# Kernel tuning notes

Measured on AMD Instinct MI355X. Metric: run time of the kernel, lower is better.

## Reference

```python
import jax, jax.numpy as jnp
import numpy as np
from jax import lax

EPS = 1e-4

def _baseconv(x, w, g, b):
    # Conv (no bias) + folded BatchNorm (per-channel scale g, shift b) + SiLU
    k = w.shape[-1]
    pad = [((k - 1) // 2, (k - 1) // 2)] * 2
    y = lax.conv_general_dilated(x, w, (1, 1), pad,
                                 dimension_numbers=('NCHW', 'OIHW', 'NCHW'))
    y = y * g[None, :, None, None] + b[None, :, None, None]
    return y * jax.nn.sigmoid(y)  # SiLU

def _block_norm(x, s):
    # Divide each of the s*s spatial sub-blocks by its global mean (over B,C,h,w)
    B, C, H, W = x.shape
    h, w = H // s, W // s
    xb = x.reshape(B, C, s, h, s, w)
    m = xb.mean(axis=(0, 1, 3, 5), keepdims=True)  # (1,1,s,1,s,1) scalar per block
    return (xb / (m + EPS)).reshape(B, C, H, W)


def setup_inputs() -> dict:
    key = jax.random.key(0)
    ks = jax.random.split(key, 8)
    B, C, H, W = 4, 128, 256, 256
    d = {}
    d['x'] = jax.random.normal(ks[0], (B, C, H, W), dtype=jnp.float32)
    def conv_w(k, cout, cin, ksz):
        return jax.random.normal(k, (cout, cin, ksz, ksz), dtype=jnp.float32) * 0.02
    # fc1/fc2/fc3: 1x1 dim->dim for SagMean scales 1,2,4
    d['w1'] = conv_w(ks[1], C, C, 1); d['g1'] = jnp.ones((C,)); d['b1'] = jnp.zeros((C,))
    d['w2'] = conv_w(ks[2], C, C, 1); d['g2'] = jnp.ones((C,)); d['b2'] = jnp.zeros((C,))
    d['w3'] = conv_w(ks[3], C, C, 1); d['g3'] = jnp.ones((C,)); d['b3'] = jnp.zeros((C,))
    # mix: 3x3 4*dim->dim
    d['wm'] = conv_w(ks[4], C, 4 * C, 3); d['gm'] = jnp.ones((C,)); d['bm'] = jnp.zeros((C,))
    # reweight mlp: two 1x1 BaseConvs (dim->dim->dim) with GELU between
    d['wa'] = conv_w(ks[5], C, C, 1); d['ga'] = jnp.ones((C,)); d['ba'] = jnp.zeros((C,))
    d['wb'] = conv_w(ks[6], C, C, 1); d['gb'] = jnp.ones((C,)); d['bb'] = jnp.zeros((C,))
    return d


def reference(x, w1, g1, b1, w2, g2, b2, w3, g3, b3, wm, gm, bm, wa, ga, ba, wb, gb, bb):
    residual = x
    x1 = jnp.maximum(x, 0.0)  # torch.max(x, tensor([0.0]))
    s1 = _baseconv(_block_norm(x1, 1), w1, g1, b1)
    s2 = _baseconv(_block_norm(x1, 2), w2, g2, b2)
    s4 = _baseconv(_block_norm(x1, 4), w3, g3, b3)
    y = jnp.concatenate([x, s1, s2, s4], axis=1)  # (B, 4C, H, W)
    y = _baseconv(y, wm, gm, bm)                  # mix 3x3 -> (B, C, H, W)
    # reweight mlp: BaseConv(SiLU) -> GELU -> BaseConv(SiLU)
    y = _baseconv(y, wa, ga, ba)
    y = jax.nn.gelu(y, approximate=False)
    y = _baseconv(y, wb, gb, bb)
    return y * residual
```

## Files before the change

### kernel.cpp

```cpp
#include <hip/hip_runtime.h>


typedef _Float16 half8 __attribute__((ext_vector_type(8)));
typedef float    f32x4 __attribute__((ext_vector_type(4)));

#define OFF_BINS 0
#define OFF_INV  256
#define OFF_WF   512
#define OFF_AMAT 164352
#define OFF_CAT  1344000
#define OFF_YMIX 269779456

__device__ __forceinline__ float silu_f(float y) { return y / (1.f + __expf(-y)); }

__device__ __forceinline__ void zero_acc(f32x4 acc[4][4]) {
#pragma unroll
  for (int mt = 0; mt < 4; ++mt)
#pragma unroll
    for (int nt = 0; nt < 4; ++nt)
#pragma unroll
      for (int r = 0; r < 4; ++r) acc[mt][nt][r] = 0.f;
}

template <int WK>
__device__ __forceinline__ void gemm_step(const _Float16* __restrict__ sM,
                                          const _Float16* __restrict__ sN,
                                          int m0, int n0, int kko, int lane,
                                          f32x4 acc[4][4]) {
  const int r15 = lane & 15;
  const int quad = lane >> 4;
  half8 a[4], b[4];
#pragma unroll
  for (int mt = 0; mt < 4; ++mt) {
    int row = m0 + mt * 16 + r15;
    a[mt] = *(const half8*)&sM[row * (WK * 8) + (((kko + quad) ^ (row & (WK - 1))) * 8)];
  }
#pragma unroll
  for (int nt = 0; nt < 4; ++nt) {
    int row = n0 + nt * 16 + r15;
    b[nt] = *(const half8*)&sN[row * (WK * 8) + (((kko + quad) ^ (row & (WK - 1))) * 8)];
  }
#pragma unroll
  for (int mt = 0; mt < 4; ++mt)
#pragma unroll
    for (int nt = 0; nt < 4; ++nt)
      acc[mt][nt] =
          __builtin_amdgcn_mfma_f32_16x16x32_f16(a[mt], b[nt], acc[mt][nt], 0, 0, 0);
}

__global__ __launch_bounds__(256) void k_prep(const float* __restrict__ w1,
                                              const float* __restrict__ w2,
                                              const float* __restrict__ w3,
                                              const float* __restrict__ wa,
                                              const float* __restrict__ wb,
                                              const float* __restrict__ wm,
                                              _Float16* __restrict__ wf16,
                                              _Float16* __restrict__ amat) {
  const float* wsrc[5] = {w1, w2, w3, wa, wb};
  const int total = 5 * 16384 + 128 * 4608;
  for (int idx = blockIdx.x * 256 + threadIdx.x; idx < total; idx += gridDim.x * 256) {
    if (idx < 81920) {
      int which = idx >> 14, o = idx & 16383;
      wf16[idx] = (_Float16)wsrc[which][o];
    } else {
      int t = idx - 81920;
      int co = t / 4608, k = t - co * 4608;
      int tap = k >> 9, ci = k & 511;
      amat[t] = (_Float16)wm[(co * 512 + ci) * 9 + tap];
    }
  }
}

__global__ __launch_bounds__(256) void k_transpose(const float* __restrict__ x,
                                                   _Float16* __restrict__ cat,
                                                   float* __restrict__ bins) {
  __shared__ float tile[64 * 132];
  __shared__ float sred[256];
  const int tid = threadIdx.x;
  const int gid = blockIdx.x;
  const int jt = gid & 3, i = (gid >> 2) & 255, b = gid >> 10;
  const int j0 = jt * 64;
  float s = 0.f;
  for (int it = 0; it < 32; ++it) {
    int lid = tid + it * 256;
    int ci = lid >> 6, px = lid & 63;
    float v = x[(b * 128 + ci) * 65536 + i * 256 + j0 + px];
    s += fmaxf(v, 0.f);
    tile[px * 132 + ci] = v;
  }
  __syncthreads();
  for (int it = 0; it < 4; ++it) {
    int lid = tid + it * 256;
    int px = lid >> 4, part = lid & 15;
    half8 h;
#pragma unroll
    for (int j = 0; j < 8; ++j) h[j] = (_Float16)tile[px * 132 + part * 8 + j];
    *(half8*)&cat[(size_t)((b * 256 + i) * 256 + j0 + px) * 512 + part * 8] = h;
  }
  sred[tid] = s;
  __syncthreads();
  for (int off = 128; off > 0; off >>= 1) {
    if (tid < off) sred[tid] += sred[tid + off];
    __syncthreads();
  }
  if (tid == 0) atomicAdd(&bins[(i >> 6) * 4 + jt], sred[0]);
}

__global__ void k_invm(const float* __restrict__ bins, float* __restrict__ inv) {
  if (threadIdx.x == 0 && blockIdx.x == 0) {
    float s4[16], tot = 0.f;
    for (int k = 0; k < 16; ++k) s4[k] = bins[k];
    for (int k = 0; k < 16; ++k) inv[5 + k] = 1.f / (s4[k] * (1.f / 2097152.f) + 1e-4f);
    for (int p = 0; p < 2; ++p)
      for (int q = 0; q < 2; ++q) {
        float s2 = s4[(2 * p) * 4 + 2 * q] + s4[(2 * p) * 4 + 2 * q + 1] +
                   s4[(2 * p + 1) * 4 + 2 * q] + s4[(2 * p + 1) * 4 + 2 * q + 1];
        tot += s2;
        inv[1 + p * 2 + q] = 1.f / (s2 * (1.f / 8388608.f) + 1e-4f);
      }
    inv[0] = 1.f / (tot * (1.f / 33554432.f) + 1e-4f);
  }
}

__global__ __launch_bounds__(256) void k1_sconv(_Float16* __restrict__ cat,
                                                const _Float16* __restrict__ wf16,
                                                const float* __restrict__ g1,
                                                const float* __restrict__ b1,
                                                const float* __restrict__ g2,
                                                const float* __restrict__ b2,
                                                const float* __restrict__ g3,
                                                const float* __restrict__ b3,
                                                const float* __restrict__ inv) {
  __shared__ _Float16 sAct[128 * 128];
  __shared__ _Float16 sW[128 * 128];
  const int tid = threadIdx.x, lane = tid & 63, wave = tid >> 6;
  const int m0 = (wave >> 1) * 64, n0 = (wave & 1) * 64;
  const int gid = blockIdx.x;
  const int jh = gid & 1, i = (gid >> 1) & 255, b = gid >> 9;
  const size_t rowbase = (size_t)((b * 256 + i) * 256 + jh * 128);

  for (int it = 0; it < 8; ++it) {
    int lid = tid + it * 256;
    int px = lid >> 4, part = lid & 15;
    half8 v = *(const half8*)&cat[(rowbase + px) * 512 + part * 8];
#pragma unroll
    for (int j = 0; j < 8; ++j) v[j] = (v[j] > (_Float16)0.f) ? v[j] : (_Float16)0.f;
    *(half8*)&sAct[px * 128 + ((part ^ (px & 15)) * 8)] = v;
  }

  const float* gs[3] = {g1, g2, g3};
  const float* bs[3] = {b1, b2, b3};
  for (int s = 0; s < 3; ++s) {
    __syncthreads();
    for (int it = 0; it < 8; ++it) {
      int lid = tid + it * 256;
      int co = lid >> 4, part = lid & 15;
      *(half8*)&sW[co * 128 + ((part ^ (co & 15)) * 8)] =
          *(const half8*)&wf16[s * 16384 + co * 128 + part * 8];
    }
    __syncthreads();
    f32x4 acc[4][4];
    zero_acc(acc);
#pragma unroll
    for (int ks = 0; ks < 4; ++ks) gemm_step<16>(sAct, sW, m0, n0, ks * 4, lane, acc);

    float a_lo, a_hi;
    if (s == 0) {
      a_lo = a_hi = inv[0];
    } else if (s == 1) {
      a_lo = a_hi = inv[1 + (i >> 7) * 2 + jh];
    } else {
      int base = 5 + (i >> 6) * 4 + jh * 2;
      a_lo = inv[base];
      a_hi = inv[base + 1];
    }
#pragma unroll
    for (int nt = 0; nt < 4; ++nt) {
      int co = n0 + nt * 16 + (lane & 15);
      float gg = gs[s][co], sh = bs[s][co];
#pragma unroll
      for (int mt = 0; mt < 4; ++mt) {
#pragma unroll
        for (int r = 0; r < 4; ++r) {
          int px = m0 + mt * 16 + (lane >> 4) * 4 + r;
          float al = (px < 64) ? a_lo : a_hi;
          float y = acc[mt][nt][r] * al * gg + sh;
          cat[(rowbase + px) * 512 + (s + 1) * 128 + co] = (_Float16)silu_f(y);
        }
      }
    }
  }
}

__global__ __launch_bounds__(256) void k2_mix(const _Float16* __restrict__ cat,
                                              const _Float16* __restrict__ amat,
                                              const float* __restrict__ gm,
                                              const float* __restrict__ bm,
                                              _Float16* __restrict__ ymix) {
  __shared__ _Float16 sAct[128 * 64];
  __shared__ _Float16 sW[128 * 64];
  const int tid = threadIdx.x, lane = tid & 63, wave = tid >> 6;
  const int m0 = (wave >> 1) * 64, n0 = (wave & 1) * 64;
  const int gid = blockIdx.x;
  const int jh = gid & 1, i = (gid >> 1) & 255, b = gid >> 9;

  f32x4 acc[4][4];
  zero_acc(acc);

  for (int tap = 0; tap < 9; ++tap) {
    const int di = tap / 3, dj = tap % 3;
    const int ii = i + di - 1;
    if (ii < 0 || ii >= 256) continue;
    const _Float16* srcRow = cat + (size_t)((b * 256 + ii) * 256) * 512;
    for (int c64 = 0; c64 < 8; ++c64) {
      const int kbase = tap * 512 + c64 * 64;
      __syncthreads();
#pragma unroll
      for (int it = 0; it < 4; ++it) {
        int lid = tid + it * 256;
        int row = lid >> 3, part = lid & 7;
        *(half8*)&sW[row * 64 + ((part ^ (row & 7)) * 8)] =
            *(const half8*)&amat[row * 4608 + kbase + part * 8];
        int jj = jh * 128 + row + dj - 1;
        half8 v;
#pragma unroll
        for (int j = 0; j < 8; ++j) v[j] = (_Float16)0.f;
        if (jj >= 0 && jj < 256)
          v = *(const half8*)&srcRow[(size_t)jj * 512 + c64 * 64 + part * 8];
        *(half8*)&sAct[row * 64 + ((part ^ (row & 7)) * 8)] = v;
      }
      __syncthreads();
      gemm_step<8>(sAct, sW, m0, n0, 0, lane, acc);
      gemm_step<8>(sAct, sW, m0, n0, 4, lane, acc);
    }
  }

  const int outbase = (b * 256 + i) * 256 + jh * 128;
#pragma unroll
  for (int nt = 0; nt < 4; ++nt) {
    int co = n0 + nt * 16 + (lane & 15);
    float gg = gm[co], sh = bm[co];
#pragma unroll
    for (int mt = 0; mt < 4; ++mt) {
#pragma unroll
      for (int r = 0; r < 4; ++r) {
        int px = m0 + mt * 16 + (lane >> 4) * 4 + r;
        float y = acc[mt][nt][r] * gg + sh;
        ymix[(size_t)(outbase + px) * 128 + co] = (_Float16)silu_f(y);
      }
    }
  }
}

__global__ __launch_bounds__(256) void k3_tail(const _Float16* __restrict__ ymix,
                                               const _Float16* __restrict__ wfa,
                                               const _Float16* __restrict__ wfb,
                                               const float* __restrict__ ga,
                                               const float* __restrict__ ba,
                                               const float* __restrict__ gb,
                                               const float* __restrict__ bbv,
                                               const float* __restrict__ x,
                                               float* __restrict__ out) {
  __shared__ _Float16 sAct[128 * 128];
  __shared__ _Float16 sW[128 * 128];
  const int tid = threadIdx.x, lane = tid & 63, wave = tid >> 6;
  const int m0 = (wave >> 1) * 64, n0 = (wave & 1) * 64;
  const int gid = blockIdx.x;
  const int jh = gid & 1, i = (gid >> 1) & 255, b = gid >> 9;
  const size_t rowbase = (size_t)((b * 256 + i) * 256 + jh * 128);

  for (int it = 0; it < 8; ++it) {
    int lid = tid + it * 256;
    int row = lid >> 4, part = lid & 15;
    *(half8*)&sAct[row * 128 + ((part ^ (row & 15)) * 8)] =
        *(const half8*)&ymix[(rowbase + row) * 128 + part * 8];
    *(half8*)&sW[row * 128 + ((part ^ (row & 15)) * 8)] =
        *(const half8*)&wfa[row * 128 + part * 8];
  }
  __syncthreads();
  f32x4 acc[4][4];
  zero_acc(acc);
#pragma unroll
  for (int ks = 0; ks < 4; ++ks) gemm_step<16>(sW, sAct, m0, n0, ks * 4, lane, acc);
  __syncthreads();

#pragma unroll
  for (int mt = 0; mt < 4; ++mt) {
#pragma unroll
    for (int r = 0; r < 4; ++r) {
      int co = m0 + mt * 16 + (lane >> 4) * 4 + r;
      float gg = ga[co], sh = ba[co];
#pragma unroll
      for (int nt = 0; nt < 4; ++nt) {
        int px = n0 + nt * 16 + (lane & 15);
        float y = acc[mt][nt][r] * gg + sh;
        float sv = silu_f(y);
        float gl = 0.5f * sv * (1.f + erff(sv * 0.70710678118f));
        sAct[px * 128 + (((co >> 3) ^ (px & 15)) * 8) + (co & 7)] = (_Float16)gl;
      }
    }
  }
  for (int it = 0; it < 8; ++it) {
    int lid = tid + it * 256;
    int co = lid >> 4, part = lid & 15;
    *(half8*)&sW[co * 128 + ((part ^ (co & 15)) * 8)] =
        *(const half8*)&wfb[co * 128 + part * 8];
  }
  __syncthreads();
  f32x4 acc2[4][4];
  zero_acc(acc2);
#pragma unroll
  for (int ks = 0; ks < 4; ++ks) gemm_step<16>(sW, sAct, m0, n0, ks * 4, lane, acc2);

#pragma unroll
  for (int mt = 0; mt < 4; ++mt) {
#pragma unroll
    for (int r = 0; r < 4; ++r) {
      int co = m0 + mt * 16 + (lane >> 4) * 4 + r;
      float gg = gb[co], sh = bbv[co];
      size_t base = (size_t)(b * 128 + co) * 65536 + i * 256 + jh * 128;
#pragma unroll
      for (int nt = 0; nt < 4; ++nt) {
        int px = n0 + nt * 16 + (lane & 15);
        float y = acc2[mt][nt][r] * gg + sh;
        out[base + px] = silu_f(y) * x[base + px];
      }
    }
  }
}

extern "C" void kernel_launch(void* const* d_in, const int* in_sizes, int n_in,
                              void* d_out, int out_size, void* d_ws, size_t ws_size,
                              hipStream_t stream) {
  (void)in_sizes; (void)n_in; (void)out_size; (void)ws_size;
  const float* x  = (const float*)d_in[0];
  const float* w1 = (const float*)d_in[1];
  const float* g1 = (const float*)d_in[2];
  const float* b1 = (const float*)d_in[3];
  const float* w2 = (const float*)d_in[4];
  const float* g2 = (const float*)d_in[5];
  const float* b2 = (const float*)d_in[6];
  const float* w3 = (const float*)d_in[7];
  const float* g3 = (const float*)d_in[8];
  const float* b3 = (const float*)d_in[9];
  const float* wm = (const float*)d_in[10];
  const float* gm = (const float*)d_in[11];
  const float* bm = (const float*)d_in[12];
  const float* wa = (const float*)d_in[13];
  const float* ga = (const float*)d_in[14];
  const float* ba = (const float*)d_in[15];
  const float* wb = (const float*)d_in[16];
  const float* gb = (const float*)d_in[17];
  const float* bb = (const float*)d_in[18];

  char* ws = (char*)d_ws;
  float*    bins = (float*)(ws + OFF_BINS);
  float*    inv  = (float*)(ws + OFF_INV);
  _Float16* wf16 = (_Float16*)(ws + OFF_WF);
  _Float16* amat = (_Float16*)(ws + OFF_AMAT);
  _Float16* cat  = (_Float16*)(ws + OFF_CAT);
  _Float16* ymix = (_Float16*)(ws + OFF_YMIX);
  float*    out  = (float*)d_out;

  hipMemsetAsync(bins, 0, 64, stream);
  k_prep<<<512, 256, 0, stream>>>(w1, w2, w3, wa, wb, wm, wf16, amat);
  k_transpose<<<4096, 256, 0, stream>>>(x, cat, bins);
  k_invm<<<1, 64, 0, stream>>>(bins, inv);
  k1_sconv<<<2048, 256, 0, stream>>>(cat, wf16, g1, b1, g2, b2, g3, b3, inv);
  k2_mix<<<2048, 256, 0, stream>>>(cat, amat, gm, bm, ymix);
  k3_tail<<<2048, 256, 0, stream>>>(ymix, wf16 + 3 * 16384, wf16 + 4 * 16384,
                                    ga, ba, gb, bb, x, out);
}
```

Baseline: 1.010 ms.

## Restructure 3x3 mix conv with shared halo rows, async LDS loads, and coalesced stores

Result: faster. 886.5 us (-12.2%).

```diff
diff --git a/kernel.cpp b/kernel.cpp
--- a/kernel.cpp
+++ b/kernel.cpp
@@ -57,16 +57,18 @@
                                               _Float16* __restrict__ wf16,
                                               _Float16* __restrict__ amat) {
   const float* wsrc[5] = {w1, w2, w3, wa, wb};
-  const int total = 5 * 16384 + 128 * 4608;
+  const int total = 81920 + 589824;
   for (int idx = blockIdx.x * 256 + threadIdx.x; idx < total; idx += gridDim.x * 256) {
     if (idx < 81920) {
       int which = idx >> 14, o = idx & 16383;
       wf16[idx] = (_Float16)wsrc[which][o];
     } else {
       int t = idx - 81920;
-      int co = t / 4608, k = t - co * 4608;
-      int tap = k >> 9, ci = k & 511;
-      amat[t] = (_Float16)wm[(co * 512 + ci) * 9 + tap];
+      int e = t & 7, ln = (t >> 3) & 63, cg = (t >> 9) & 7;
+      int kc = (t >> 12) & 15, tap = t >> 16;
+      int co = cg * 16 + (ln & 15);
+      int kl = kc * 32 + (ln >> 4) * 8 + e;
+      amat[t] = (_Float16)wm[(co * 512 + kl) * 9 + tap];
     }
   }
 }
@@ -174,6 +176,7 @@
       a_lo = inv[base];
       a_hi = inv[base + 1];
     }
+    __syncthreads();
 #pragma unroll
     for (int nt = 0; nt < 4; ++nt) {
       int co = n0 + nt * 16 + (lane & 15);
@@ -185,10 +188,45 @@
           int px = m0 + mt * 16 + (lane >> 4) * 4 + r;
           float al = (px < 64) ? a_lo : a_hi;
           float y = acc[mt][nt][r] * al * gg + sh;
-          cat[(rowbase + px) * 512 + (s + 1) * 128 + co] = (_Float16)silu_f(y);
+          sW[px * 128 + (((co >> 3) ^ (px & 15)) * 8) + (co & 7)] = (_Float16)silu_f(y);
         }
       }
     }
+    __syncthreads();
+    for (int it = 0; it < 8; ++it) {
+      int lid = tid + it * 256;
+      int px = lid >> 4, o = lid & 15;
+      half8 v = *(half8*)&sW[px * 128 + ((o ^ (px & 15)) * 8)];
+      *(half8*)&cat[(rowbase + px) * 512 + (s + 1) * 128 + o * 8] = v;
+    }
+  }
+}
+
+__device__ __forceinline__ void k2_stage(const _Float16* __restrict__ cat,
+                                         _Float16* __restrict__ buf,
+                                         int b, int ii, int jh, int c64,
+                                         int lane, int wave) {
+  const _Float16* src = cat + (size_t)((b * 256 + ii) * 256) * 512 + c64 * 64;
+  const int rsub = lane >> 3, l7 = lane & 7;
+#pragma unroll
+  for (int it = 0; it < 4; ++it) {
+    int rb = (wave * 4 + it) * 8;
+    int row = rb + rsub;
+    int j = jh * 128 + row - 1;
+    int part = l7 ^ (row & 7);
+    if ((unsigned)j < 256u)
+      __builtin_amdgcn_global_load_lds(
+          (const __attribute__((address_space(1))) void*)(src + (size_t)j * 512 + part * 8),
+          (__attribute__((address_space(3))) void*)(buf + rb * 64), 16, 0, 0);
+  }
+  if (wave == 3) {
+    int row = 128 + rsub;
+    int j = jh * 128 + row - 1;
+    int part = l7 ^ (row & 7);
+    if (lane < 16 && (unsigned)j < 256u)
+      __builtin_amdgcn_global_load_lds(
+          (const __attribute__((address_space(1))) void*)(src + (size_t)j * 512 + part * 8),
+          (__attribute__((address_space(3))) void*)(buf + 128 * 64), 16, 0, 0);
   }
 }
 
@@ -197,58 +235,88 @@
                                               const float* __restrict__ gm,
                                               const float* __restrict__ bm,
                                               _Float16* __restrict__ ymix) {
-  __shared__ _Float16 sAct[128 * 64];
-  __shared__ _Float16 sW[128 * 64];
+  __shared__ _Float16 sAct[2][132 * 64];
   const int tid = threadIdx.x, lane = tid & 63, wave = tid >> 6;
   const int m0 = (wave >> 1) * 64, n0 = (wave & 1) * 64;
   const int gid = blockIdx.x;
   const int jh = gid & 1, i = (gid >> 1) & 255, b = gid >> 9;
 
+  if (tid < 16) {
+    int ez = (jh == 0) ? 0 : 129;
+    half8 z = {};
+    *(half8*)&sAct[tid >> 3][ez * 64 + (tid & 7) * 8] = z;
+  }
+
+  int dits[3], nd = 0;
+#pragma unroll
+  for (int dit = 0; dit < 3; ++dit) {
+    int ii = i - 1 + dit;
+    if (ii >= 0 && ii < 256) dits[nd++] = dit;
+  }
+  const int nst = nd * 8;
+
+  k2_stage(cat, sAct[0], b, i - 1 + dits[0], jh, 0, lane, wave);
+
   f32x4 acc[4][4];
   zero_acc(acc);
-
-  for (int tap = 0; tap < 9; ++tap) {
-    const int di = tap / 3, dj = tap % 3;
-    const int ii = i + di - 1;
-    if (ii < 0 || ii >= 256) continue;
-    const _Float16* srcRow = cat + (size_t)((b * 256 + ii) * 256) * 512;
-    for (int c64 = 0; c64 < 8; ++c64) {
-      const int kbase = tap * 512 + c64 * 64;
-      __syncthreads();
-#pragma unroll
-      for (int it = 0; it < 4; ++it) {
-        int lid = tid + it * 256;
-        int row = lid >> 3, part = lid & 7;
-        *(half8*)&sW[row * 64 + ((part ^ (row & 7)) * 8)] =
-            *(const half8*)&amat[row * 4608 + kbase + part * 8];
-        int jj = jh * 128 + row + dj - 1;
-        half8 v;
-#pragma unroll
-        for (int j = 0; j < 8; ++j) v[j] = (_Float16)0.f;
-        if (jj >= 0 && jj < 256)
-          v = *(const half8*)&srcRow[(size_t)jj * 512 + c64 * 64 + part * 8];
-        *(half8*)&sAct[row * 64 + ((part ^ (row & 7)) * 8)] = v;
-      }
-      __syncthreads();
-      gemm_step<8>(sAct, sW, m0, n0, 0, lane, acc);
-      gemm_step<8>(sAct, sW, m0, n0, 4, lane, acc);
-    }
-  }
-
+  const int r15 = lane & 15, quad = lane >> 4;
+  const int cg0 = n0 >> 4;
+
+  for (int s = 0; s < nst; ++s) {
+    __syncthreads();
+    if (s + 1 < nst)
+      k2_stage(cat, sAct[(s + 1) & 1], b, i - 1 + dits[(s + 1) >> 3], jh,
+               (s + 1) & 7, lane, wave);
+    const int dit = dits[s >> 3], c64 = s & 7;
+    const _Float16* buf = sAct[s & 1];
+#pragma unroll
+    for (int dj = 0; dj < 3; ++dj) {
+      const int tap = dit * 3 + dj;
+#pragma unroll
+      for (int kcl = 0; kcl < 2; ++kcl) {
+        const _Float16* bb =
+            amat + ((((size_t)(tap * 16 + c64 * 2 + kcl)) * 8 + cg0) * 64 + lane) * 8;
+        half8 a[4], bf[4];
+#pragma unroll
+        for (int nt = 0; nt < 4; ++nt) bf[nt] = *(const half8*)&bb[nt * 512];
+#pragma unroll
+        for (int mt = 0; mt < 4; ++mt) {
+          int row = m0 + mt * 16 + r15 + dj;
+          a[mt] = *(const half8*)&buf[row * 64 + (((kcl * 4 + quad) ^ (row & 7)) * 8)];
+        }
+#pragma unroll
+        for (int mt = 0; mt < 4; ++mt)
+#pragma unroll
+          for (int nt = 0; nt < 4; ++nt)
+            acc[mt][nt] = __builtin_amdgcn_mfma_f32_16x16x32_f16(a[mt], bf[nt],
+                                                                 acc[mt][nt], 0, 0, 0);
+      }
+    }
+  }
+
+  __syncthreads();
+  _Float16* scratch = &sAct[0][0];
   const int outbase = (b * 256 + i) * 256 + jh * 128;
 #pragma unroll
   for (int nt = 0; nt < 4; ++nt) {
-    int co = n0 + nt * 16 + (lane & 15);
+    int co = n0 + nt * 16 + r15;
     float gg = gm[co], sh = bm[co];
 #pragma unroll
-    for (int mt = 0; mt < 4; ++mt) {
+    for (int mt = 0; mt < 4; ++mt)
 #pragma unroll
       for (int r = 0; r < 4; ++r) {
-        int px = m0 + mt * 16 + (lane >> 4) * 4 + r;
+        int px = m0 + mt * 16 + quad * 4 + r;
         float y = acc[mt][nt][r] * gg + sh;
-        ymix[(size_t)(outbase + px) * 128 + co] = (_Float16)silu_f(y);
-      }
-    }
+        scratch[px * 128 + (((co >> 3) ^ (px & 15)) * 8) + (co & 7)] =
+            (_Float16)silu_f(y);
+      }
+  }
+  __syncthreads();
+  for (int it = 0; it < 8; ++it) {
+    int lid = tid + it * 256;
+    int px = lid >> 4, o = lid & 15;
+    half8 v = *(half8*)&scratch[px * 128 + ((o ^ (px & 15)) * 8)];
+    *(half8*)&ymix[(size_t)(outbase + px) * 128 + o * 8] = v;
   }
 }
 
```
